# Kernel tuning notes

Measured on AMD Instinct MI355X. Metric: run time of the kernel, lower is better.

## Reference

```python
import jax, jax.numpy as jnp
import numpy as np

IMG_H = IMG_W = 14
HEADS = 8
HEAD_DIM = 32
INNER = HEADS * HEAD_DIM  # 256
IN_CH = 384
OUT_CH = 768
HIDDEN = 4 * IN_CH  # 1536
SCALE = HEAD_DIM ** -0.5
EPS = 1e-5


def _relative_index(h, w):
    # static numpy computation, identical to the torch buffer
    yy, xx = np.meshgrid(np.arange(h), np.arange(w), indexing='ij')
    coords = np.stack([yy.ravel(), xx.ravel()])            # [2, N]
    rel = coords[:, :, None] - coords[:, None, :]          # [2, N, N]
    rel[0] += h - 1
    rel[1] += w - 1
    rel[0] *= 2 * w - 1
    return (rel[0] + rel[1]).reshape(-1)                   # [N*N]


def _maxpool3s2p1(x):
    # torch MaxPool2d(3, 2, 1): pad with -inf
    return jax.lax.reduce_window(
        x, -jnp.inf, jax.lax.max,
        window_dimensions=(1, 1, 3, 3),
        window_strides=(1, 1, 2, 2),
        padding=((0, 0), (0, 0), (1, 1), (1, 1)))


def _layernorm(x, g, b):
    mu = jnp.mean(x, axis=-1, keepdims=True)
    var = jnp.mean(jnp.square(x - mu), axis=-1, keepdims=True)
    return (x - mu) * jax.lax.rsqrt(var + EPS) * g + b


def setup_inputs() -> dict:
    key = jax.random.key(0)
    ks = jax.random.split(key, 12)
    s = 0.02
    return {
        'x': jax.random.normal(ks[0], (64, IN_CH, 28, 28), jnp.float32),
        'W_qkv': jax.random.normal(ks[1], (IN_CH, 3 * INNER), jnp.float32) * s,
        'bias_table': jax.random.normal(ks[2], ((2 * IMG_H - 1) * (2 * IMG_W - 1), HEADS), jnp.float32) * s,
        'W_out': jax.random.normal(ks[3], (INNER, OUT_CH), jnp.float32) * s,
        'b_out': jnp.zeros((OUT_CH,), jnp.float32),
        'ln1_g': jnp.ones((IN_CH,), jnp.float32),
        'ln1_b': jnp.zeros((IN_CH,), jnp.float32),
        'ln2_g': jnp.ones((OUT_CH,), jnp.float32),
        'ln2_b': jnp.zeros((OUT_CH,), jnp.float32),
        'W_fc1': jax.random.normal(ks[4], (OUT_CH, HIDDEN), jnp.float32) * s,
        'b_fc1': jnp.zeros((HIDDEN,), jnp.float32),
        'W_fc2': jax.random.normal(ks[5], (HIDDEN, OUT_CH), jnp.float32) * s,
        'b_fc2': jnp.zeros((OUT_CH,), jnp.float32),
        'W_proj': jax.random.normal(ks[6], (OUT_CH, IN_CH), jnp.float32) * s,
    }


def reference(x, W_qkv, bias_table, W_out, b_out, ln1_g, ln1_b, ln2_g, ln2_b,
              W_fc1, b_fc1, W_fc2, b_fc2, W_proj):
    B = x.shape[0]
    N = IMG_H * IMG_W
    rel_idx = jnp.asarray(_relative_index(IMG_H, IMG_W))   # [N*N]

    # --- downsample branch ---
    xp = _maxpool3s2p1(x)                                  # [B, Cin, 14, 14]
    proj = jnp.einsum('bchw,oc->bohw', xp, W_proj)         # 1x1 conv, no bias

    # --- attention branch ---
    xa = _maxpool3s2p1(x)                                  # [B, Cin, 14, 14]
    tokens = xa.reshape(B, IN_CH, N).transpose(0, 2, 1)    # [B, N, Cin]
    tokens = _layernorm(tokens, ln1_g, ln1_b)
    qkv = tokens @ W_qkv                                   # [B, N, 3*INNER]
    q, k, v = jnp.split(qkv, 3, axis=-1)
    def heads(t):
        return t.reshape(B, N, HEADS, HEAD_DIM).transpose(0, 2, 1, 3)  # [B,H,N,D]
    q, k, v = heads(q), heads(k), heads(v)
    dots = jnp.einsum('bhid,bhjd->bhij', q, k) * SCALE     # [B,H,N,N]
    bias = bias_table[rel_idx].reshape(N, N, HEADS).transpose(2, 0, 1)  # [H,N,N]
    attn = jax.nn.softmax(dots + bias[None], axis=-1)
    out = jnp.einsum('bhij,bhjd->bhid', attn, v)           # [B,H,N,D]
    out = out.transpose(0, 2, 1, 3).reshape(B, N, INNER)
    out = out @ W_out + b_out                              # [B, N, Cout]
    attn_map = out.transpose(0, 2, 1).reshape(B, OUT_CH, IMG_H, IMG_W)

    h = proj + attn_map                                    # [B, Cout, 14, 14]

    # --- feed-forward branch ---
    t = h.reshape(B, OUT_CH, N).transpose(0, 2, 1)         # [B, N, Cout]
    t = _layernorm(t, ln2_g, ln2_b)
    t = jax.nn.gelu(t @ W_fc1 + b_fc1, approximate=False)
    t = t @ W_fc2 + b_fc2
    ffn = t.transpose(0, 2, 1).reshape(B, OUT_CH, IMG_H, IMG_W)

    return h + ffn
```

## Files before the change

kernel.cpp:

```cpp
#include <hip/hip_runtime.h>
#include <hip/hip_bf16.h>
#include <cmath>

typedef unsigned short ushortT;
typedef unsigned int u32;
typedef __attribute__((ext_vector_type(8))) short short8;
typedef __attribute__((ext_vector_type(4))) float floatx4;

#define IMG 14
#define NTOK 196
#define BATCH 64
#define M_TOT 12544
#define M_HALF 6272
#define INCH 384
#define OUTCH 768
#define HIDDEN 1536
#define HEADS 8
#define HDIM 32
#define SCALE 0.17677669529663687f

__device__ __forceinline__ float b2f(ushortT u) {
    union { u32 i; float f; } v; v.i = ((u32)u) << 16; return v.f;
}
__device__ __forceinline__ ushortT f2b(float f) {
    union { float f; u32 i; } v; v.f = f;
    u32 r = v.i + 0x7FFFu + ((v.i >> 16) & 1u);
    return (ushortT)(r >> 16);
}

__device__ __forceinline__ void async_ld16(const void* g, void* l) {
    __builtin_amdgcn_global_load_lds(
        (const __attribute__((address_space(1))) u32*)g,
        (__attribute__((address_space(3))) u32*)l, 16, 0, 0);
}

__global__ __launch_bounds__(256) void prep_pool(
    const float* __restrict__ Wqkv, const float* __restrict__ Wout,
    const float* __restrict__ Wfc1, const float* __restrict__ Wfc2,
    const float* __restrict__ Wproj, const float* __restrict__ x,
    const float* __restrict__ bias_tb,
    ushortT* __restrict__ oQkv, ushortT* __restrict__ oOut,
    ushortT* __restrict__ oFc1, ushortT* __restrict__ oFc2,
    ushortT* __restrict__ oProj, ushortT* __restrict__ pooled,
    float* __restrict__ bias_exp) {
    __shared__ __align__(16) char lds_raw[26880];
    int blk = blockIdx.x;
    int tid = threadIdx.x;
    if (blk >= 4608) {
        int idx4 = (blk - 4608) * 256 + tid;
        int h = idx4 / 10816;
        int rem = idx4 - h * 10816;
        int i = rem / 52;
        int j0 = (rem - i * 52) * 4;
        float v[4];
        #pragma unroll
        for (int u = 0; u < 4; ++u) {
            int j = j0 + u;
            float val = 0.f;
            if (i < 196 && j < 196) {
                int iy = i / 14, ix = i - iy * 14;
                int jy = j / 14, jx = j - jy * 14;
                val = bias_tb[((iy - jy + 13) * 27 + (ix - jx + 13)) * 8 + h];
            }
            v[u] = val;
        }
        *(float4*)(bias_exp + (size_t)idx4 * 4) = *(const float4*)v;
        return;
    }
    if (blk >= 3072) {
        int pblk = blk - 3072;
        int cg = pblk % 24, b = pblk / 24;
        float* hm = (float*)lds_raw;
        const float* xsrc = x + ((size_t)b * INCH + cg * 16) * 784;
        for (int t = tid; t < 448; t += 256) {
            int c = t / 28, hrow = t - c * 28;
            const float* rp = xsrc + c * 784 + hrow * 28;
            float r[28];
            #pragma unroll
            for (int u = 0; u < 7; ++u)
                *(float4*)(r + u * 4) = *(const float4*)(rp + u * 4);
            float* hr = hm + (size_t)t * 15;
            #pragma unroll
            for (int j = 0; j < 14; ++j) {
                float a = j ? r[2 * j - 1] : r[0];
                hr[j] = fmaxf(fmaxf(a, r[2 * j]), r[2 * j + 1]);
            }
        }
        __syncthreads();
        for (int chunk = tid; chunk < NTOK * 2; chunk += 256) {
            int n = chunk >> 1, q = chunk & 1;
            int hh = n / IMG, ww = n - hh * IMG;
            int ya = hh ? 2 * hh - 1 : 0;
            int y1 = 2 * hh, y2 = 2 * hh + 1;
            ushortT o[8];
            #pragma unroll
            for (int cc = 0; cc < 8; ++cc) {
                const float* base = hm + (size_t)(q * 8 + cc) * 28 * 15 + ww;
                float mv = fmaxf(fmaxf(base[ya * 15], base[y1 * 15]), base[y2 * 15]);
                o[cc] = f2b(mv);
            }
            *(uint4*)(pooled + ((size_t)b * NTOK + n) * INCH + cg * 16 + q * 8) =
                *(const uint4*)o;
        }
        return;
    }
    if (blk >= 2784) {
        int i = ((blk - 2784) * 256 + tid) * 4;
        float4 v = *(const float4*)(Wproj + i);
        ushortT o[4] = { f2b(v.x), f2b(v.y), f2b(v.z), f2b(v.w) };
        *(uint2*)(oProj + i) = *(const uint2*)o;
        return;
    }
    const float* in; ushortT* out; int R, C, tile;
    if (blk < 288)       { in = Wqkv; out = oQkv; R = 384;  C = 768;  tile = blk; }
    else if (blk < 480)  { in = Wout; out = oOut; R = 256;  C = 768;  tile = blk - 288; }
    else if (blk < 1632) { in = Wfc1; out = oFc1; R = 768;  C = 1536; tile = blk - 480; }
    else                 { in = Wfc2; out = oFc2; R = 1536; C = 768;  tile = blk - 1632; }
    int tilesX = C >> 5;
    int bx = (tile % tilesX) * 32, by = (tile / tilesX) * 32;
    ushortT (*t)[33] = (ushortT (*)[33])lds_raw;
    int tx = tid & 31, ty = tid >> 5;
    #pragma unroll
    for (int i = 0; i < 4; ++i) {
        int r = by + ty * 4 + i;
        t[ty * 4 + i][tx] = f2b(in[(size_t)r * C + bx + tx]);
    }
    __syncthreads();
    #pragma unroll
    for (int i = 0; i < 4; ++i) {
        int r = bx + ty * 4 + i;
        out[(size_t)r * R + by + tx] = t[tx][ty * 4 + i];
    }
}

template <int VE>
__global__ __launch_bounds__(256) void ln_kernel(const ushortT* __restrict__ in,
                                                 const float* __restrict__ gw,
                                                 const float* __restrict__ bw,
                                                 ushortT* __restrict__ out) {
    constexpr int C = 192 * VE;
    int wave = threadIdx.x >> 6, lane = threadIdx.x & 63;
    int m = blockIdx.x * 4 + wave;
    const ushortT* row = in + (size_t)m * C;
    float v[3][VE];
    float s = 0.f, q = 0.f;
    #pragma unroll
    for (int seg = 0; seg < 3; ++seg) {
        int idx = seg * 64 * VE + lane * VE;
        ushortT tmp[VE];
        if constexpr (VE == 2) *(u32*)tmp = *(const u32*)(row + idx);
        else                   *(uint2*)tmp = *(const uint2*)(row + idx);
        #pragma unroll
        for (int k = 0; k < VE; ++k) {
            float f = b2f(tmp[k]);
            v[seg][k] = f;
            s += f;
            q += f * f;
        }
    }
    #pragma unroll
    for (int off = 32; off > 0; off >>= 1) {
        s += __shfl_xor(s, off, 64);
        q += __shfl_xor(q, off, 64);
    }
    float mu = s / (float)C;
    float var = q / (float)C - mu * mu;
    float rs = rsqrtf(var + 1e-5f);
    #pragma unroll
    for (int seg = 0; seg < 3; ++seg) {
        int idx = seg * 64 * VE + lane * VE;
        float g[VE], bb[VE];
        if constexpr (VE == 2) {
            *(float2*)g = *(const float2*)(gw + idx);
            *(float2*)bb = *(const float2*)(bw + idx);
        } else {
            *(float4*)g = *(const float4*)(gw + idx);
            *(float4*)bb = *(const float4*)(bw + idx);
        }
        ushortT o[VE];
        #pragma unroll
        for (int k = 0; k < VE; ++k)
            o[k] = f2b((v[seg][k] - mu) * rs * g[k] + bb[k]);
        if constexpr (VE == 2) *(u32*)(out + (size_t)m * C + idx) = *(const u32*)o;
        else                   *(uint2*)(out + (size_t)m * C + idx) = *(const uint2*)o;
    }
}

__global__ __launch_bounds__(256) void attn_kernel(const ushortT* __restrict__ qkv,
                                                   const float* __restrict__ bias_exp,
                                                   ushortT* __restrict__ attn_out) {
    int bh = blockIdx.x;
    int b = bh >> 3, h = bh & 7;
    __shared__ ushortT Qs[208 * 32];
    __shared__ ushortT Ks[208 * 32];
    __shared__ ushortT Vts[32 * 232];
    __shared__ ushortT Ps[4][16 * 232];
    const int tid = threadIdx.x, wave = tid >> 6, lane = tid & 63;

    const uint4* q4 = (const uint4*)(qkv + (size_t)bh * 6272);
    const uint4* k4 = (const uint4*)(qkv + (size_t)(512 + bh) * 6272);
    const uint4* v4 = (const uint4*)(qkv + (size_t)(1024 + bh) * 6272);
    uint4* Q4 = (uint4*)Qs;
    uint4* K4 = (uint4*)Ks;
    for (int t = tid; t < 784; t += 256) { Q4[t] = q4[t]; K4[t] = k4[t]; }
    const uint4 z4 = {0, 0, 0, 0};
    for (int t = tid; t < 48; t += 256) { Q4[784 + t] = z4; K4[784 + t] = z4; }
    for (int t = tid; t < 784; t += 256) {
        int j = t >> 2, d0 = (t & 3) * 8;
        uint4 v = v4[t];
        const ushortT* vs = (const ushortT*)&v;
        #pragma unroll
        for (int u = 0; u < 8; ++u)
            Vts[(d0 + u) * 232 + j] = vs[u];
    }
    for (int t = tid; t < 1152; t += 256) {
        int d = t / 36, j = 196 + t - d * 36;
        Vts[d * 232 + j] = 0;
    }
    for (int t = tid; t < 1536; t += 256) {
        int w = t / 384, rem = t - w * 384;
        int row = rem / 24, j = 208 + rem - (rem / 24) * 24;
        Ps[w][row * 232 + j] = 0;
    }
    __syncthreads();

    const int fr = (lane & 15), fk = (lane >> 4) * 8;
    short8 kf[13];
    #pragma unroll
    for (int nt = 0; nt < 13; ++nt)
        kf[nt] = *(const short8*)(Ks + (nt * 16 + fr) * 32 + fk);

    const int i0r = (lane >> 4) * 4;
    const int colL = lane & 15;
    ushortT* Pw = &Ps[wave][0];

    for (int mt = wave; mt < 13; mt += 4) {
        short8 af = *(const short8*)(Qs + (mt * 16 + fr) * 32 + fk);
        floatx4 sc[13];
        #pragma unroll
        for (int nt = 0; nt < 13; ++nt)
            sc[nt] = __builtin_amdgcn_mfma_f32_16x16x32_bf16(
                af, kf[nt], (floatx4){0.f, 0.f, 0.f, 0.f}, 0, 0, 0);

        float rsum[4] = {0.f, 0.f, 0.f, 0.f};
        const float* bb = bias_exp + ((size_t)h * 208 + mt * 16 + i0r) * 208 + colL;
        #pragma unroll
        for (int nt = 0; nt < 13; ++nt) {
            #pragma unroll
            for (int r = 0; r < 4; ++r) {
                float bias = bb[r * 208 + nt * 16];
                float p = __expf(sc[nt][r] * SCALE + bias);
                if (nt == 12 && colL >= 4) p = 0.f;
                rsum[r] += p;
                Pw[(i0r + r) * 232 + nt * 16 + colL] = f2b(p);
            }
        }
        #pragma unroll
        for (int off = 1; off < 16; off <<= 1) {
            #pragma unroll
            for (int r = 0; r < 4; ++r) rsum[r] += __shfl_xor(rsum[r], off, 64);
        }

        floatx4 o[2];
        o[0] = (floatx4){0.f, 0.f, 0.f, 0.f};
        o[1] = (floatx4){0.f, 0.f, 0.f, 0.f};
        #pragma unroll
        for (int kt = 0; kt < 7; ++kt) {
            short8 pf = *(const short8*)(Pw + fr * 232 + kt * 32 + fk);
            #pragma unroll
            for (int n2 = 0; n2 < 2; ++n2) {
                short8 vf = *(const short8*)(Vts + (n2 * 16 + fr) * 232 + kt * 32 + fk);
                o[n2] = __builtin_amdgcn_mfma_f32_16x16x32_bf16(pf, vf, o[n2], 0, 0, 0);
            }
        }
        float invl[4];
        #pragma unroll
        for (int r = 0; r < 4; ++r) invl[r] = 1.f / rsum[r];
        #pragma unroll
        for (int n2 = 0; n2 < 2; ++n2) {
            #pragma unroll
            for (int r = 0; r < 4; ++r) {
                int i = mt * 16 + i0r + r;
                if (i < 196)
                    attn_out[((size_t)(b * 196 + i)) * 256 + h * 32 + n2 * 16 + colL] =
                        f2b(o[n2][r] * invl[r]);
            }
        }
    }
}

template <int EPI, typename OUT_T>
__global__ __launch_bounds__(256) void gemm128(
    const ushortT* __restrict__ A1, const ushortT* __restrict__ B1, int K1,
    const ushortT* __restrict__ A2, const ushortT* __restrict__ B2, int K2,
    const float* __restrict__ bias, const ushortT* __restrict__ addend,
    OUT_T* __restrict__ out, int m_off) {
    __shared__ ushortT As[128 * 32];
    __shared__ ushortT Bs[128 * 32];
    const int tid = threadIdx.x, wave = tid >> 6, lane = tid & 63;
    const int wr = (wave >> 1) * 64;
    const int wc = (wave & 1) * 64;
    const int tm = blockIdx.x, tn = blockIdx.y;

    floatx4 acc[4][4];
    #pragma unroll
    for (int a = 0; a < 4; ++a)
        #pragma unroll
        for (int c = 0; c < 4; ++c)
            acc[a][c] = (floatx4){0.f, 0.f, 0.f, 0.f};

    const int fr = lane & 15, fk = (lane >> 4) * 8;

    auto stage = [&](const ushortT* G, int ld, int row0, int k0, ushortT* S) {
        #pragma unroll
        for (int i = 0; i < 2; ++i) {
            int c = tid + i * 256;
            async_ld16(G + (size_t)(row0 + (c >> 2)) * ld + k0 + (c & 3) * 8, S + c * 8);
        }
    };

    auto kloop = [&](const ushortT* A, const ushortT* B, int K) {
        for (int k0 = 0; k0 < K; k0 += 32) {
            stage(A, K, tm * 128, k0, As);
            stage(B, K, tn * 128, k0, Bs);
            __syncthreads();
            short8 af[4], bf[4];
            #pragma unroll
            for (int mt = 0; mt < 4; ++mt)
                af[mt] = *(const short8*)(As + (wr + mt * 16 + fr) * 32 + fk);
            #pragma unroll
            for (int nt = 0; nt < 4; ++nt)
                bf[nt] = *(const short8*)(Bs + (wc + nt * 16 + fr) * 32 + fk);
            #pragma unroll
            for (int mt = 0; mt < 4; ++mt)
                #pragma unroll
                for (int nt = 0; nt < 4; ++nt)
                    acc[mt][nt] = __builtin_amdgcn_mfma_f32_16x16x32_bf16(
                        af[mt], bf[nt], acc[mt][nt], 0, 0, 0);
            __syncthreads();
        }
    };

    kloop(A1, B1, K1);
    if (B2) kloop(A2, B2, K2);

    const int nb = tn * 128 + wc + (lane & 15);
    const int mbl = wr + ((lane >> 4) << 2);
    #pragma unroll
    for (int nt = 0; nt < 4; ++nt) {
        int n = nb + nt * 16;
        float bv = (EPI == 0) ? 0.f : bias[n];
        #pragma unroll
        for (int mt = 0; mt < 4; ++mt) {
            #pragma unroll
            for (int r = 0; r < 4; ++r) {
                int m = tm * 128 + mbl + mt * 16 + r;
                float v = acc[mt][nt][r] + bv;
                if constexpr (EPI == 0) {
                    int bb = m / 196, tok = m - bb * 196;
                    int reg = n >> 8, head = (n >> 5) & 7, d = n & 31;
                    out[((size_t)((reg * 512 + bb * 8 + head) * 196 + tok)) * 32 + d] = f2b(v);
                } else if constexpr (EPI == 1) {
                    out[(size_t)m * 768 + n] = f2b(v);
                } else if constexpr (EPI == 2) {
                    float gl = 0.5f * v * (1.f + erff(v * 0.70710678118654752f));
                    out[(size_t)m * 1536 + n] = f2b(gl);
                } else {
                    v += b2f(addend[(size_t)m * 768 + n]);
                    int mg = m + m_off;
                    int bb = mg / 196, tok = mg - bb * 196;
                    out[((size_t)(bb * 768 + n)) * 196 + tok] = v;
                }
            }
        }
    }
}

extern "C" void kernel_launch(void* const* d_in, const int* in_sizes, int n_in,
                              void* d_out, int out_size, void* d_ws, size_t ws_size,
                              hipStream_t stream) {
    const float* x       = (const float*)d_in[0];
    const float* W_qkv   = (const float*)d_in[1];
    const float* bias_tb = (const float*)d_in[2];
    const float* W_out   = (const float*)d_in[3];
    const float* b_out   = (const float*)d_in[4];
    const float* ln1_g   = (const float*)d_in[5];
    const float* ln1_b   = (const float*)d_in[6];
    const float* ln2_g   = (const float*)d_in[7];
    const float* ln2_b   = (const float*)d_in[8];
    const float* W_fc1   = (const float*)d_in[9];
    const float* b_fc1   = (const float*)d_in[10];
    const float* W_fc2   = (const float*)d_in[11];
    const float* b_fc2   = (const float*)d_in[12];
    const float* W_proj  = (const float*)d_in[13];
    float* out = (float*)d_out;

    char* ws = (char*)d_ws;
    ushortT* pooled = (ushortT*)(ws);
    ushortT* tln1   = (ushortT*)(ws + 9633792);
    ushortT* attno  = tln1;
    ushortT* qkvb   = (ushortT*)(ws + 19267584);
    ushortT* tln2   = qkvb;
    ushortT* mid    = (ushortT*)(ws);
    ushortT* htok   = (ushortT*)(ws + 38535168);
    float*   bias_exp = (float*)(ws + 38535168);
    ushortT* wTqkv  = (ushortT*)(ws + 57802752);
    ushortT* wTout  = wTqkv + 768 * 384;
    ushortT* wTfc1  = wTout + 768 * 256;
    ushortT* wTfc2  = wTfc1 + 1536 * 768;
    ushortT* wProjB = wTfc2 + 768 * 1536;
    const size_t weights_end = 57802752 +
        (size_t)(768 * 384 + 768 * 256 + 1536 * 768 + 768 * 1536 + 768 * 384) * 2;
    const bool ffn_full = ws_size >= weights_end + (size_t)M_TOT * HIDDEN * 2;
    ushortT* midf = (ushortT*)(ws + weights_end);

    prep_pool<<<4946, 256, 0, stream>>>(W_qkv, W_out, W_fc1, W_fc2, W_proj, x, bias_tb,
                                        wTqkv, wTout, wTfc1, wTfc2, wProjB, pooled,
                                        bias_exp);

    ln_kernel<2><<<M_TOT / 4, 256, 0, stream>>>(pooled, ln1_g, ln1_b, tln1);

    gemm128<0, ushortT><<<dim3(98, 6), 256, 0, stream>>>(tln1, wTqkv, 384,
                                                nullptr, nullptr, 0,
                                                nullptr, nullptr, qkvb, 0);
    attn_kernel<<<512, 256, 0, stream>>>(qkvb, bias_exp, attno);

    gemm128<1, ushortT><<<dim3(98, 6), 256, 0, stream>>>(attno, wTout, 256,
                                                pooled, wProjB, 384,
                                                b_out, nullptr, htok, 0);
    ln_kernel<4><<<M_TOT / 4, 256, 0, stream>>>(htok, ln2_g, ln2_b, tln2);

    if (ffn_full) {
        gemm128<2, ushortT><<<dim3(98, 12), 256, 0, stream>>>(tln2, wTfc1, 768,
                                                     nullptr, nullptr, 0,
                                                     b_fc1, nullptr, midf, 0);
        gemm128<3, float><<<dim3(98, 6), 256, 0, stream>>>(midf, wTfc2, 1536,
                                                    nullptr, nullptr, 0,
                                                    b_fc2, htok, out, 0);
    } else {
        for (int half = 0; half < 2; ++half) {
            const ushortT* a2 = tln2 + (size_t)half * M_HALF * 768;
            gemm128<2, ushortT><<<dim3(49, 12), 256, 0, stream>>>(a2, wTfc1, 768,
                                                         nullptr, nullptr, 0,
                                                         b_fc1, nullptr, mid, 0);
            gemm128<3, float><<<dim3(49, 6), 256, 0, stream>>>(mid, wTfc2, 1536,
                                                        nullptr, nullptr, 0,
                                                        b_fc2, htok + (size_t)half * M_HALF * 768,
                                                        out, half * M_HALF);
        }
    }
    (void)in_sizes; (void)n_in; (void)out_size; (void)ws_size;
}
```

Baseline: 422.5 us.

## Double-buffer GEMM LDS staging and move projection GEMM into QKV launch

Rewrites the shared GEMM core to double-buffer its LDS tiles, so the next k-slice loads while the current one feeds the MFMAs, and it drops one barrier per step. The pooled-input projection GEMM is split out of the out-projection kernel and run in the same launch as the QKV GEMM, writing its result straight into the output tensor. Later epilogues then read, accumulate and write that output with float4 accesses instead of carrying a bf16 addend. This adds read-modify-write traffic on the fp32 output, needs twice the LDS, and relies on four-row groups never crossing a 196-token batch boundary for the float4 stores.

```diff
diff --git a/kernel.cpp b/kernel.cpp
--- a/kernel.cpp
+++ b/kernel.cpp
@@ -289,18 +289,67 @@
     }
 }
 
-template <int EPI, typename OUT_T>
-__global__ __launch_bounds__(256) void gemm128(
-    const ushortT* __restrict__ A1, const ushortT* __restrict__ B1, int K1,
-    const ushortT* __restrict__ A2, const ushortT* __restrict__ B2, int K2,
-    const float* __restrict__ bias, const ushortT* __restrict__ addend,
-    OUT_T* __restrict__ out, int m_off) {
-    __shared__ ushortT As[128 * 32];
-    __shared__ ushortT Bs[128 * 32];
+__device__ __forceinline__ void gemm_core128(
+    const ushortT* __restrict__ A, const ushortT* __restrict__ B, int K,
+    int tm, int tn, ushortT* As, ushortT* Bs,
+    floatx4 (&acc)[4][4], int tid, int wave, int lane) {
+    const int fr = lane & 15, fk = (lane >> 4) * 8;
+    const int wr = (wave >> 1) * 64, wc = (wave & 1) * 64;
+    auto stage = [&](int buf, int k0) {
+        const ushortT* Ag = A + (size_t)(tm * 128) * K + k0;
+        const ushortT* Bg = B + (size_t)(tn * 128) * K + k0;
+        ushortT* Al = As + buf * 4096;
+        ushortT* Bl = Bs + buf * 4096;
+        #pragma unroll
+        for (int i = 0; i < 2; ++i) {
+            int c = tid + i * 256;
+            async_ld16(Ag + (size_t)(c >> 2) * K + (c & 3) * 8, Al + c * 8);
+        }
+        #pragma unroll
+        for (int i = 0; i < 2; ++i) {
+            int c = tid + i * 256;
+            async_ld16(Bg + (size_t)(c >> 2) * K + (c & 3) * 8, Bl + c * 8);
+        }
+    };
+    const int nsteps = K >> 5;
+    stage(0, 0);
+    int cur = 0;
+    for (int t = 0; t < nsteps; ++t) {
+        __syncthreads();
+        if (t + 1 < nsteps) stage(cur ^ 1, (t + 1) * 32);
+        const ushortT* Ab = As + cur * 4096;
+        const ushortT* Bb = Bs + cur * 4096;
+        short8 af[4], bf[4];
+        #pragma unroll
+        for (int mt = 0; mt < 4; ++mt)
+            af[mt] = *(const short8*)(Ab + (wr + mt * 16 + fr) * 32 + fk);
+        #pragma unroll
+        for (int nt = 0; nt < 4; ++nt)
+            bf[nt] = *(const short8*)(Bb + (wc + nt * 16 + fr) * 32 + fk);
+        #pragma unroll
+        for (int mt = 0; mt < 4; ++mt)
+            #pragma unroll
+            for (int nt = 0; nt < 4; ++nt)
+                acc[mt][nt] = __builtin_amdgcn_mfma_f32_16x16x32_bf16(
+                    af[mt], bf[nt], acc[mt][nt], 0, 0, 0);
+        cur ^= 1;
+    }
+}
+
+__global__ __launch_bounds__(256) void gemm_qkvproj(
+    const ushortT* __restrict__ tln1, const ushortT* __restrict__ wTqkv,
+    const ushortT* __restrict__ pooled, const ushortT* __restrict__ wProjB,
+    const float* __restrict__ b_out, ushortT* __restrict__ qkvb,
+    float* __restrict__ outT) {
+    __shared__ ushortT As[2 * 4096];
+    __shared__ ushortT Bs[2 * 4096];
     const int tid = threadIdx.x, wave = tid >> 6, lane = tid & 63;
-    const int wr = (wave >> 1) * 64;
-    const int wc = (wave & 1) * 64;
-    const int tm = blockIdx.x, tn = blockIdx.y;
+    const int tm = blockIdx.x;
+    const int y = blockIdx.y;
+    const bool isP = y >= 6;
+    const int tn = isP ? y - 6 : y;
+    const ushortT* A = isP ? pooled : tln1;
+    const ushortT* B = isP ? wProjB : wTqkv;
 
     floatx4 acc[4][4];
     #pragma unroll
@@ -309,68 +358,104 @@
         for (int c = 0; c < 4; ++c)
             acc[a][c] = (floatx4){0.f, 0.f, 0.f, 0.f};
 
-    const int fr = lane & 15, fk = (lane >> 4) * 8;
-
-    auto stage = [&](const ushortT* G, int ld, int row0, int k0, ushortT* S) {
-        #pragma unroll
-        for (int i = 0; i < 2; ++i) {
-            int c = tid + i * 256;
-            async_ld16(G + (size_t)(row0 + (c >> 2)) * ld + k0 + (c & 3) * 8, S + c * 8);
-        }
-    };
-
-    auto kloop = [&](const ushortT* A, const ushortT* B, int K) {
-        for (int k0 = 0; k0 < K; k0 += 32) {
-            stage(A, K, tm * 128, k0, As);
-            stage(B, K, tn * 128, k0, Bs);
-            __syncthreads();
-            short8 af[4], bf[4];
-            #pragma unroll
-            for (int mt = 0; mt < 4; ++mt)
-                af[mt] = *(const short8*)(As + (wr + mt * 16 + fr) * 32 + fk);
-            #pragma unroll
-            for (int nt = 0; nt < 4; ++nt)
-                bf[nt] = *(const short8*)(Bs + (wc + nt * 16 + fr) * 32 + fk);
-            #pragma unroll
-            for (int mt = 0; mt < 4; ++mt)
-                #pragma unroll
-                for (int nt = 0; nt < 4; ++nt)
-                    acc[mt][nt] = __builtin_amdgcn_mfma_f32_16x16x32_bf16(
-                        af[mt], bf[nt], acc[mt][nt], 0, 0, 0);
-            __syncthreads();
-        }
-    };
-
-    kloop(A1, B1, K1);
-    if (B2) kloop(A2, B2, K2);
-
+    gemm_core128(A, B, 384, tm, tn, As, Bs, acc, tid, wave, lane);
+
+    const int wr = (wave >> 1) * 64, wc = (wave & 1) * 64;
     const int nb = tn * 128 + wc + (lane & 15);
     const int mbl = wr + ((lane >> 4) << 2);
+    if (!isP) {
+        #pragma unroll
+        for (int nt = 0; nt < 4; ++nt) {
+            int n = nb + nt * 16;
+            int reg = n >> 8, head = (n >> 5) & 7, d = n & 31;
+            #pragma unroll
+            for (int mt = 0; mt < 4; ++mt) {
+                #pragma unroll
+                for (int r = 0; r < 4; ++r) {
+                    int m = tm * 128 + mbl + mt * 16 + r;
+                    int bb = m / 196, tok = m - bb * 196;
+                    qkvb[((size_t)((reg * 512 + bb * 8 + head) * 196 + tok)) * 32 + d] =
+                        f2b(acc[mt][nt][r]);
+                }
+            }
+        }
+    } else {
+        #pragma unroll
+        for (int nt = 0; nt < 4; ++nt) {
+            int n = nb + nt * 16;
+            float bv = b_out[n];
+            #pragma unroll
+            for (int mt = 0; mt < 4; ++mt) {
+                int m0 = tm * 128 + mbl + mt * 16;
+                int bb = m0 / 196, tok = m0 - bb * 196;
+                float vv[4];
+                #pragma unroll
+                for (int r = 0; r < 4; ++r) vv[r] = acc[mt][nt][r] + bv;
+                *(float4*)(outT + ((size_t)(bb * 768 + n)) * 196 + tok) =
+                    *(const float4*)vv;
+            }
+        }
+    }
+}
+
+template <int EPI>
+__global__ __launch_bounds__(256) void gemm128p(
+    const ushortT* __restrict__ A, const ushortT* __restrict__ B, int K,
+    const float* __restrict__ bias, ushortT* __restrict__ outb,
+    float* __restrict__ outT, int m_off) {
+    __shared__ ushortT As[2 * 4096];
+    __shared__ ushortT Bs[2 * 4096];
+    const int tid = threadIdx.x, wave = tid >> 6, lane = tid & 63;
+    const int tm = blockIdx.x, tn = blockIdx.y;
+
+    floatx4 acc[4][4];
+    #pragma unroll
+    for (int a = 0; a < 4; ++a)
+        #pragma unroll
+        for (int c = 0; c < 4; ++c)
+            acc[a][c] = (floatx4){0.f, 0.f, 0.f, 0.f};
+
+    gemm_core128(A, B, K, tm, tn, As, Bs, acc, tid, wave, lane);
+
+    const int wr = (wave >> 1) * 64, wc = (wave & 1) * 64;
+    const int nb = tn * 128 + wc + (lane & 15);
+    const int mbl = wr + ((lane >> 4) << 2);
     #pragma unroll
     for (int nt = 0; nt < 4; ++nt) {
         int n = nb + nt * 16;
-        float bv = (EPI == 0) ? 0.f : bias[n];
+        float bv = (EPI == 2 || EPI == 3) ? bias[n] : 0.f;
         #pragma unroll
         for (int mt = 0; mt < 4; ++mt) {
-            #pragma unroll
-            for (int r = 0; r < 4; ++r) {
-                int m = tm * 128 + mbl + mt * 16 + r;
-                float v = acc[mt][nt][r] + bv;
-                if constexpr (EPI == 0) {
-                    int bb = m / 196, tok = m - bb * 196;
-                    int reg = n >> 8, head = (n >> 5) & 7, d = n & 31;
-                    out[((size_t)((reg * 512 + bb * 8 + head) * 196 + tok)) * 32 + d] = f2b(v);
-                } else if constexpr (EPI == 1) {
-                    out[(size_t)m * 768 + n] = f2b(v);
-                } else if constexpr (EPI == 2) {
+            int m0 = tm * 128 + mbl + mt * 16;
+            if constexpr (EPI == 1) {
+                int bb = m0 / 196, tok = m0 - bb * 196;
+                float* p = outT + ((size_t)(bb * 768 + n)) * 196 + tok;
+                float hv[4];
+                *(float4*)hv = *(const float4*)p;
+                float vv[4];
+                #pragma unroll
+                for (int r = 0; r < 4; ++r) vv[r] = acc[mt][nt][r] + hv[r];
+                *(float4*)p = *(const float4*)vv;
+                #pragma unroll
+                for (int r = 0; r < 4; ++r)
+                    outb[(size_t)(m0 + r) * 768 + n] = f2b(vv[r]);
+            } else if constexpr (EPI == 2) {
+                #pragma unroll
+                for (int r = 0; r < 4; ++r) {
+                    float v = acc[mt][nt][r] + bv;
                     float gl = 0.5f * v * (1.f + erff(v * 0.70710678118654752f));
-                    out[(size_t)m * 1536 + n] = f2b(gl);
-                } else {
-                    v += b2f(addend[(size_t)m * 768 + n]);
-                    int mg = m + m_off;
-                    int bb = mg / 196, tok = mg - bb * 196;
-                    out[((size_t)(bb * 768 + n)) * 196 + tok] = v;
+                    outb[(size_t)(m0 + r) * 1536 + n] = f2b(gl);
                 }
+            } else {
+                int mg = m0 + m_off;
+                int bb = mg / 196, tok = mg - bb * 196;
+                float* p = outT + ((size_t)(bb * 768 + n)) * 196 + tok;
+                float hv[4];
+                *(float4*)hv = *(const float4*)p;
+                float vv[4];
+                #pragma unroll
+                for (int r = 0; r < 4; ++r) vv[r] = acc[mt][nt][r] + bv + hv[r];
+                *(float4*)p = *(const float4*)vv;
             }
         }
     }
@@ -420,33 +505,27 @@
 
     ln_kernel<2><<<M_TOT / 4, 256, 0, stream>>>(pooled, ln1_g, ln1_b, tln1);
 
-    gemm128<0, ushortT><<<dim3(98, 6), 256, 0, stream>>>(tln1, wTqkv, 384,
-                                                nullptr, nullptr, 0,
-                                                nullptr, nullptr, qkvb, 0);
+    gemm_qkvproj<<<dim3(98, 12), 256, 0, stream>>>(tln1, wTqkv, pooled, wProjB,
+                                                   b_out, qkvb, out);
     attn_kernel<<<512, 256, 0, stream>>>(qkvb, bias_exp, attno);
 
-    gemm128<1, ushortT><<<dim3(98, 6), 256, 0, stream>>>(attno, wTout, 256,
-                                                pooled, wProjB, 384,
-                                                b_out, nullptr, htok, 0);
+    gemm128p<1><<<dim3(98, 6), 256, 0, stream>>>(attno, wTout, 256,
+                                                 nullptr, htok, out, 0);
     ln_kernel<4><<<M_TOT / 4, 256, 0, stream>>>(htok, ln2_g, ln2_b, tln2);
 
     if (ffn_full) {
-        gemm128<2, ushortT><<<dim3(98, 12), 256, 0, stream>>>(tln2, wTfc1, 768,
-                                                     nullptr, nullptr, 0,
-                                                     b_fc1, nullptr, midf, 0);
-        gemm128<3, float><<<dim3(98, 6), 256, 0, stream>>>(midf, wTfc2, 1536,
-                                                    nullptr, nullptr, 0,
-                                                    b_fc2, htok, out, 0);
+        gemm128p<2><<<dim3(98, 12), 256, 0, stream>>>(tln2, wTfc1, 768,
+                                                      b_fc1, midf, nullptr, 0);
+        gemm128p<3><<<dim3(98, 6), 256, 0, stream>>>(midf, wTfc2, 1536,
+                                                     b_fc2, nullptr, out, 0);
     } else {
         for (int half = 0; half < 2; ++half) {
             const ushortT* a2 = tln2 + (size_t)half * M_HALF * 768;
-            gemm128<2, ushortT><<<dim3(49, 12), 256, 0, stream>>>(a2, wTfc1, 768,
-                                                         nullptr, nullptr, 0,
-                                                         b_fc1, nullptr, mid, 0);
-            gemm128<3, float><<<dim3(49, 6), 256, 0, stream>>>(mid, wTfc2, 1536,
-                                                        nullptr, nullptr, 0,
-                                                        b_fc2, htok + (size_t)half * M_HALF * 768,
-                                                        out, half * M_HALF);
+            gemm128p<2><<<dim3(49, 12), 256, 0, stream>>>(a2, wTfc1, 768,
+                                                          b_fc1, mid, nullptr, 0);
+            gemm128p<3><<<dim3(49, 6), 256, 0, stream>>>(mid, wTfc2, 1536,
+                                                         b_fc2, nullptr, out,
+                                                         half * M_HALF);
         }
     }
     (void)in_sizes; (void)n_in; (void)out_size; (void)ws_size;
```

After: 402.6 us. -4.7%, faster.
